# Optimization experiments

Hardware: AMD Instinct MI355X
Metric: run time of the kernel (lower is better)

## Reference

```python
import jax, jax.numpy as jnp
import numpy as np

NUM_TREES = 100
TREE_DEPTH = 5
INPUT_DIM = 256
NUM_CLASSES = 64
BATCH = 8192
NUM_NODES = 2 ** TREE_DEPTH - 1   # 31 decision nodes per tree
NUM_LEAVES = 2 ** TREE_DEPTH      # 32 leaves per tree


def setup_inputs() -> dict:
    key = jax.random.key(0)
    k_x, k_w, k_b, k_l = jax.random.split(key, 4)
    x = jax.random.normal(k_x, (BATCH, INPUT_DIM), dtype=jnp.float32)
    # stacked per-tree decision-node params (torch.randn init)
    node_w = jax.random.normal(k_w, (NUM_TREES, NUM_NODES, INPUT_DIM), dtype=jnp.float32)
    node_b = jax.random.normal(k_b, (NUM_TREES, NUM_NODES), dtype=jnp.float32)
    leaves = jax.random.normal(k_l, (NUM_TREES, NUM_LEAVES, NUM_CLASSES), dtype=jnp.float32)
    return {"x": x, "node_w": node_w, "node_b": node_b, "leaves": leaves}


def reference(x, node_w, node_b, leaves):
    # x: [B, D]; node_w: [T, Nn, D]; node_b: [T, Nn]; leaves: [T, Nl, C]
    T = node_w.shape[0]
    B = x.shape[0]
    depth = int(np.log2(leaves.shape[1]))
    idx = jnp.zeros((T, B), dtype=jnp.int32)
    for _ in range(depth):  # small fixed depth loop
        # gather each sample's routing node per tree: [T, B, D] and [T, B]
        w_g = jnp.take_along_axis(node_w, idx[:, :, None], axis=1)
        b_g = jnp.take_along_axis(node_b, idx, axis=1)
        decisions = jax.nn.sigmoid(jnp.einsum('tbd,bd->tb', w_g, x) + b_g)
        idx = 2 * idx + (decisions <= 0.5).astype(jnp.int32)
    # leaf gather: [T, B, C], then forest average over trees -> [B, C]
    tree_preds = jnp.take_along_axis(leaves, idx[:, :, None], axis=1)
    return jnp.mean(tree_preds, axis=0)
```

## Files before the change

kernel.cpp:

```cpp
#include <hip/hip_runtime.h>


typedef __bf16 bf16;
typedef __attribute__((ext_vector_type(8))) __bf16 bf16x8;
typedef __attribute__((ext_vector_type(4))) float f32x4;
typedef __attribute__((ext_vector_type(4))) unsigned int u32x4;

#define NTREES 100
#define NB     8192
#define ND     256
#define NNODES 31
#define NLEAF  32
#define NCLS   64
#define TAU    2.0e-3f

static __device__ __forceinline__ void gload16(const void* g, void* l) {
    __builtin_amdgcn_global_load_lds(
        (const __attribute__((address_space(1))) void*)g,
        (__attribute__((address_space(3))) void*)l, 16, 0, 0);
}

static __device__ __forceinline__ void split8(const f32x4 v0, const f32x4 v1,
                                              bf16x8* hi, bf16x8* lo) {
    u32x4 b0 = __builtin_bit_cast(u32x4, v0);
    u32x4 b1 = __builtin_bit_cast(u32x4, v1);
    u32x4 h0 = b0 & 0xFFFF0000u;
    u32x4 h1 = b1 & 0xFFFF0000u;
    f32x4 r0 = v0 - __builtin_bit_cast(f32x4, h0);
    f32x4 r1 = v1 - __builtin_bit_cast(f32x4, h1);
    u32x4 c0 = __builtin_bit_cast(u32x4, r0);
    u32x4 c1 = __builtin_bit_cast(u32x4, r1);
    u32x4 hp, lp;
    hp[0] = __builtin_amdgcn_perm(b0[1], b0[0], 0x07060302u);
    hp[1] = __builtin_amdgcn_perm(b0[3], b0[2], 0x07060302u);
    hp[2] = __builtin_amdgcn_perm(b1[1], b1[0], 0x07060302u);
    hp[3] = __builtin_amdgcn_perm(b1[3], b1[2], 0x07060302u);
    lp[0] = __builtin_amdgcn_perm(c0[1], c0[0], 0x07060302u);
    lp[1] = __builtin_amdgcn_perm(c0[3], c0[2], 0x07060302u);
    lp[2] = __builtin_amdgcn_perm(c1[1], c1[0], 0x07060302u);
    lp[3] = __builtin_amdgcn_perm(c1[3], c1[2], 0x07060302u);
    *hi = __builtin_bit_cast(bf16x8, hp);
    *lo = __builtin_bit_cast(bf16x8, lp);
}

static __device__ __forceinline__ int traverse(const float z[16], float* mn_out) {
    float a0 = z[0];
    bool d0 = a0 <= 0.f;
    float a1 = d0 ? z[1] : z[0];
    bool d1 = a1 <= 0.f;
    float a2 = d0 ? (d1 ? z[3] : z[2]) : (d1 ? z[1] : z[0]);
    bool d2 = a2 <= 0.f;
    float m0 = d2 ? z[1] : z[0], m1 = d2 ? z[3] : z[2];
    float m2 = d2 ? z[5] : z[4], m3 = d2 ? z[7] : z[6];
    float p0 = d1 ? m1 : m0, p1 = d1 ? m3 : m2;
    float a3 = d0 ? p1 : p0;
    bool d3 = a3 <= 0.f;
    float n0 = d3 ? z[1] : z[0],  n1 = d3 ? z[3] : z[2];
    float n2 = d3 ? z[5] : z[4],  n3 = d3 ? z[7] : z[6];
    float n4 = d3 ? z[9] : z[8],  n5 = d3 ? z[11] : z[10];
    float n6 = d3 ? z[13] : z[12], n7 = d3 ? z[15] : z[14];
    float q0 = d2 ? n1 : n0, q1 = d2 ? n3 : n2;
    float q2 = d2 ? n5 : n4, q3 = d2 ? n7 : n6;
    float r0 = d1 ? q1 : q0, r1 = d1 ? q3 : q2;
    float a4 = d0 ? r1 : r0;
    bool d4 = a4 <= 0.f;
    *mn_out = fminf(fminf(fminf(fabsf(a0), fabsf(a1)),
                          fminf(fabsf(a2), fabsf(a3))), fabsf(a4));
    return ((int)d0 << 4) | ((int)d1 << 3) | ((int)d2 << 2)
         | ((int)d3 << 1) | (int)d4;
}

__global__ void prep(const float* __restrict__ wf, const float* __restrict__ lv,
                     bf16* __restrict__ wimg, bf16* __restrict__ lv16) {
    if (blockIdx.x < 208) {
        int i = blockIdx.x * 256 + threadIdx.x;
        int oct_g = i & 31;
        int row   = (i >> 5) & 127;
        int tg    = i >> 12;
        int tree  = tg * 8 + (row >> 4), node = row & 15;
        bf16x8 h8, l8;
        if (tree < NTREES) {
            const float* src = wf + ((size_t)tree * NNODES + node) * ND + oct_g * 8;
#pragma unroll
            for (int e = 0; e < 8; ++e) {
                float f = src[e];
                bf16 h = (bf16)f;
                h8[e] = h;
                l8[e] = (bf16)(f - (float)h);
            }
        } else {
#pragma unroll
            for (int e = 0; e < 8; ++e) { h8[e] = (bf16)0.f; l8[e] = (bf16)0.f; }
        }
        int kq = oct_g >> 3, oct = oct_g & 7, cp = oct ^ (row & 7);
        size_t b = (size_t)tg * 65536 + (size_t)kq * 16384 + row * 64 + cp * 8;
        *(bf16x8*)(wimg + b)        = h8;
        *(bf16x8*)(wimg + b + 8192) = l8;
    } else {
        int i = (blockIdx.x - 208) * 256 + threadIdx.x;
        lv16[i] = (bf16)lv[i];
    }
}

__global__ __launch_bounds__(256, 2) void forest_all(
    const float* __restrict__ x,
    const bf16* __restrict__ wimg,
    const float* __restrict__ wf,
    const float* __restrict__ bias,
    unsigned char* __restrict__ idxb)
{
    __shared__ char lds[65536];

    const int tid  = threadIdx.x;
    const int wave = tid >> 6;
    const int lane = tid & 63;
    const int m    = lane & 15;
    const int q    = lane >> 4;

    const int lin  = blockIdx.x + gridDim.x * blockIdx.y;
    const int xcd  = lin & 7;
    const int slot = lin >> 3;
    const int mg   = xcd * 4 + (slot / 13);
    const int tg   = slot % 13;

    f32x4 acc[4][8];
#pragma unroll
    for (int mi = 0; mi < 4; ++mi)
#pragma unroll
        for (int ni = 0; ni < 8; ++ni)
            acc[mi][ni] = (f32x4){0.f, 0.f, 0.f, 0.f};

    const float* xbase = x + (size_t)(mg * 256 + wave * 64 + m) * ND + q * 8;
    const bf16* wsrc = wimg + (size_t)tg * 65536;

#pragma unroll
    for (int j = 0; j < 8; ++j) {
        int idx = j * 256 + tid;
        gload16(wsrc + idx * 8, lds + idx * 16);
    }
    f32x4 raw[4][2];
#pragma unroll
    for (int mi = 0; mi < 4; ++mi) {
        raw[mi][0] = *(const f32x4*)(xbase + mi * 4096);
        raw[mi][1] = *(const f32x4*)(xbase + mi * 4096 + 4);
    }
    __syncthreads();

#pragma unroll
    for (int kq = 0; kq < 4; ++kq) {
        const bf16* bufc = (const bf16*)(lds + (kq & 1) * 32768);
        if (kq < 3) {
            char* bufn = lds + ((kq + 1) & 1) * 32768;
#pragma unroll
            for (int j = 0; j < 8; ++j) {
                int idx = j * 256 + tid;
                gload16(wsrc + (size_t)(kq + 1) * 16384 + idx * 8, bufn + idx * 16);
            }
        }
#pragma unroll
        for (int kkq = 0; kkq < 2; ++kkq) {
            const int kk = kq * 2 + kkq;
            bf16x8 cah[4], cal[4];
#pragma unroll
            for (int mi = 0; mi < 4; ++mi)
                split8(raw[mi][0], raw[mi][1], &cah[mi], &cal[mi]);
            if (kk < 7) {
#pragma unroll
                for (int mi = 0; mi < 4; ++mi) {
                    raw[mi][0] = *(const f32x4*)(xbase + mi * 4096 + (kk + 1) * 32);
                    raw[mi][1] = *(const f32x4*)(xbase + mi * 4096 + (kk + 1) * 32 + 4);
                }
            }
#pragma unroll
            for (int ni = 0; ni < 8; ++ni) {
                const int n  = ni * 16 + m;
                const int cp = (kkq * 4 + q) ^ (m & 7);
                bf16x8 bh = *(const bf16x8*)(bufc + n * 64 + cp * 8);
                bf16x8 bl = *(const bf16x8*)(bufc + 8192 + n * 64 + cp * 8);
#pragma unroll
                for (int mi = 0; mi < 4; ++mi) {
                    acc[mi][ni] = __builtin_amdgcn_mfma_f32_16x16x32_bf16(cal[mi], bh, acc[mi][ni], 0, 0, 0);
                    acc[mi][ni] = __builtin_amdgcn_mfma_f32_16x16x32_bf16(cah[mi], bl, acc[mi][ni], 0, 0, 0);
                    acc[mi][ni] = __builtin_amdgcn_mfma_f32_16x16x32_bf16(cah[mi], bh, acc[mi][ni], 0, 0, 0);
                }
            }
        }
        __syncthreads();
    }

    float biasv[8];
#pragma unroll
    for (int ni = 0; ni < 8; ++ni) {
        int tree = tg * 8 + ni;
        biasv[ni] = (tree < NTREES) ? bias[(size_t)tree * NNODES + m] : 0.f;
    }

    float* ws_ = (float*)lds + wave * 1280;
    const int sg = mg * 256 + wave * 64 + lane;
    unsigned int pk0 = 0, pk1 = 0;
#pragma unroll
    for (int ni = 0; ni < 8; ++ni) {
#pragma unroll
        for (int mi = 0; mi < 4; ++mi)
#pragma unroll
            for (int r = 0; r < 4; ++r)
                ws_[(mi * 16 + q * 4 + r) * 20 + m] = acc[mi][ni][r] + biasv[ni];
        f32x4 z0 = *(f32x4*)&ws_[lane * 20];
        f32x4 z1 = *(f32x4*)&ws_[lane * 20 + 4];
        f32x4 z2 = *(f32x4*)&ws_[lane * 20 + 8];
        f32x4 z3 = *(f32x4*)&ws_[lane * 20 + 12];
        float z[16] = {z0[0], z0[1], z0[2], z0[3], z1[0], z1[1], z1[2], z1[3],
                       z2[0], z2[1], z2[2], z2[3], z3[0], z3[1], z3[2], z3[3]};
        float mn;
        int leaf = traverse(z, &mn);
        const int tree = tg * 8 + ni;
        if (tree < NTREES && mn < TAU) {
            const float* xr = x + (size_t)sg * ND;
            float zc[16];
#pragma unroll
            for (int nd = 0; nd < 16; ++nd) zc[nd] = z[nd];
#pragma unroll
            for (int nd = 0; nd < 16; ++nd) {
                if (fabsf(z[nd]) < TAU) {
                    const float* wr = wf + ((size_t)tree * NNODES + nd) * ND;
                    double s0 = 0.0, s1 = 0.0;
#pragma unroll 4
                    for (int k2 = 0; k2 < 32; ++k2) {
                        f32x4 xv = *(const f32x4*)(xr + k2 * 8);
                        f32x4 wv = *(const f32x4*)(wr + k2 * 8);
                        f32x4 xu = *(const f32x4*)(xr + k2 * 8 + 4);
                        f32x4 wu = *(const f32x4*)(wr + k2 * 8 + 4);
                        s0 += (double)xv[0] * wv[0] + (double)xv[1] * wv[1]
                            + (double)xv[2] * wv[2] + (double)xv[3] * wv[3];
                        s1 += (double)xu[0] * wu[0] + (double)xu[1] * wu[1]
                            + (double)xu[2] * wu[2] + (double)xu[3] * wu[3];
                    }
                    double zt = s0 + s1 + (double)bias[(size_t)tree * NNODES + nd];
                    zc[nd] = (zt <= 0.0) ? -1.f : 1.f;
                }
            }
            float mn2;
            leaf = traverse(zc, &mn2);
        }
        if (ni < 4) pk0 |= (unsigned)leaf << (8 * ni);
        else        pk1 |= (unsigned)leaf << (8 * (ni - 4));
    }
    unsigned char* dst = idxb + (size_t)sg * NTREES + tg * 8;
    *(unsigned int*)dst = pk0;
    if (tg < 12) *(unsigned int*)(dst + 4) = pk1;
}

__global__ void leaf_gather(const unsigned char* __restrict__ idxb,
                            const bf16* __restrict__ lv16,
                            float* __restrict__ out) {
    const int wave = threadIdx.x >> 6;
    const int lane = threadIdx.x & 63;
    const int s = blockIdx.x * 4 + wave;
    unsigned int rw = 0;
    if (lane < 25) rw = *(const unsigned int*)(idxb + (size_t)s * NTREES + lane * 4);
    float acc = 0.f;
#pragma unroll 10
    for (int t = 0; t < NTREES; ++t) {
        unsigned int wrd = __shfl(rw, t >> 2);
        int li = (wrd >> ((t & 3) * 8)) & 255;
        acc += (float)lv16[((size_t)t * NLEAF + li) * NCLS + lane];
    }
    out[(size_t)s * NCLS + lane] = acc * 0.01f;
}

extern "C" void kernel_launch(void* const* d_in, const int* in_sizes, int n_in,
                              void* d_out, int out_size, void* d_ws, size_t ws_size,
                              hipStream_t stream) {
    const float* x  = (const float*)d_in[0];
    const float* nw = (const float*)d_in[1];
    const float* nb = (const float*)d_in[2];
    const float* lv = (const float*)d_in[3];
    float* out = (float*)d_out;

    char* ws = (char*)d_ws;
    bf16* wimg = (bf16*)(ws + 0);
    unsigned char* idxb = (unsigned char*)(ws + 1703936);
    bf16* lv16 = (bf16*)(ws + 2523136);
    if (ws_size < (size_t)2932736) return;

    prep<<<1008, 256, 0, stream>>>(nw, lv, wimg, lv16);
    forest_all<<<dim3(13, 32), 256, 0, stream>>>(x, wimg, nw, nb, idxb);
    leaf_gather<<<NB / 4, 256, 0, stream>>>(idxb, lv16, out);
}
```

Measured before the change: 118.8 us.

## Shrink forest tile to four trees per block to raise occupancy

Each forest_all block now handles 4 trees instead of 8, so 100 trees split evenly into 25 groups with no padded tree. The grid grows to 25x32, and LDS per block and accumulator registers are halved, so three blocks can fit per CU. The software prefetch of x into registers is dropped and x is loaded directly before each split. The cost is that x is loaded and split twice as many times across blocks, and there is no longer any latency hiding for the x loads.

```diff
diff --git a/kernel.cpp b/kernel.cpp
--- a/kernel.cpp
+++ b/kernel.cpp
@@ -72,44 +72,39 @@
 
 __global__ void prep(const float* __restrict__ wf, const float* __restrict__ lv,
                      bf16* __restrict__ wimg, bf16* __restrict__ lv16) {
-    if (blockIdx.x < 208) {
+    if (blockIdx.x < 200) {
         int i = blockIdx.x * 256 + threadIdx.x;
         int oct_g = i & 31;
-        int row   = (i >> 5) & 127;
-        int tg    = i >> 12;
-        int tree  = tg * 8 + (row >> 4), node = row & 15;
+        int row   = (i >> 5) & 63;
+        int tg    = i >> 11;
+        int tree  = tg * 4 + (row >> 4), node = row & 15;
+        const float* src = wf + ((size_t)tree * NNODES + node) * ND + oct_g * 8;
         bf16x8 h8, l8;
-        if (tree < NTREES) {
-            const float* src = wf + ((size_t)tree * NNODES + node) * ND + oct_g * 8;
-#pragma unroll
-            for (int e = 0; e < 8; ++e) {
-                float f = src[e];
-                bf16 h = (bf16)f;
-                h8[e] = h;
-                l8[e] = (bf16)(f - (float)h);
-            }
-        } else {
-#pragma unroll
-            for (int e = 0; e < 8; ++e) { h8[e] = (bf16)0.f; l8[e] = (bf16)0.f; }
+#pragma unroll
+        for (int e = 0; e < 8; ++e) {
+            float f = src[e];
+            bf16 h = (bf16)f;
+            h8[e] = h;
+            l8[e] = (bf16)(f - (float)h);
         }
         int kq = oct_g >> 3, oct = oct_g & 7, cp = oct ^ (row & 7);
-        size_t b = (size_t)tg * 65536 + (size_t)kq * 16384 + row * 64 + cp * 8;
+        size_t b = (size_t)tg * 32768 + (size_t)kq * 8192 + row * 64 + cp * 8;
         *(bf16x8*)(wimg + b)        = h8;
-        *(bf16x8*)(wimg + b + 8192) = l8;
+        *(bf16x8*)(wimg + b + 4096) = l8;
     } else {
-        int i = (blockIdx.x - 208) * 256 + threadIdx.x;
+        int i = (blockIdx.x - 200) * 256 + threadIdx.x;
         lv16[i] = (bf16)lv[i];
     }
 }
 
-__global__ __launch_bounds__(256, 2) void forest_all(
+__global__ __launch_bounds__(256, 3) void forest_all(
     const float* __restrict__ x,
     const bf16* __restrict__ wimg,
     const float* __restrict__ wf,
     const float* __restrict__ bias,
     unsigned char* __restrict__ idxb)
 {
-    __shared__ char lds[65536];
+    __shared__ char lds[32768];
 
     const int tid  = threadIdx.x;
     const int wave = tid >> 6;
@@ -120,41 +115,35 @@
     const int lin  = blockIdx.x + gridDim.x * blockIdx.y;
     const int xcd  = lin & 7;
     const int slot = lin >> 3;
-    const int mg   = xcd * 4 + (slot / 13);
-    const int tg   = slot % 13;
-
-    f32x4 acc[4][8];
+    const int mg   = xcd * 4 + (slot / 25);
+    const int tg   = slot % 25;
+
+    f32x4 acc[4][4];
 #pragma unroll
     for (int mi = 0; mi < 4; ++mi)
 #pragma unroll
-        for (int ni = 0; ni < 8; ++ni)
+        for (int ni = 0; ni < 4; ++ni)
             acc[mi][ni] = (f32x4){0.f, 0.f, 0.f, 0.f};
 
     const float* xbase = x + (size_t)(mg * 256 + wave * 64 + m) * ND + q * 8;
-    const bf16* wsrc = wimg + (size_t)tg * 65536;
-
-#pragma unroll
-    for (int j = 0; j < 8; ++j) {
+    const bf16* wsrc = wimg + (size_t)tg * 32768;
+
+#pragma unroll
+    for (int j = 0; j < 4; ++j) {
         int idx = j * 256 + tid;
         gload16(wsrc + idx * 8, lds + idx * 16);
     }
-    f32x4 raw[4][2];
-#pragma unroll
-    for (int mi = 0; mi < 4; ++mi) {
-        raw[mi][0] = *(const f32x4*)(xbase + mi * 4096);
-        raw[mi][1] = *(const f32x4*)(xbase + mi * 4096 + 4);
-    }
     __syncthreads();
 
 #pragma unroll
     for (int kq = 0; kq < 4; ++kq) {
-        const bf16* bufc = (const bf16*)(lds + (kq & 1) * 32768);
+        const bf16* bufc = (const bf16*)(lds + (kq & 1) * 16384);
         if (kq < 3) {
-            char* bufn = lds + ((kq + 1) & 1) * 32768;
-#pragma unroll
-            for (int j = 0; j < 8; ++j) {
+            char* bufn = lds + ((kq + 1) & 1) * 16384;
+#pragma unroll
+            for (int j = 0; j < 4; ++j) {
                 int idx = j * 256 + tid;
-                gload16(wsrc + (size_t)(kq + 1) * 16384 + idx * 8, bufn + idx * 16);
+                gload16(wsrc + (size_t)(kq + 1) * 8192 + idx * 8, bufn + idx * 16);
             }
         }
 #pragma unroll
@@ -162,21 +151,17 @@
             const int kk = kq * 2 + kkq;
             bf16x8 cah[4], cal[4];
 #pragma unroll
-            for (int mi = 0; mi < 4; ++mi)
-                split8(raw[mi][0], raw[mi][1], &cah[mi], &cal[mi]);
-            if (kk < 7) {
-#pragma unroll
-                for (int mi = 0; mi < 4; ++mi) {
-                    raw[mi][0] = *(const f32x4*)(xbase + mi * 4096 + (kk + 1) * 32);
-                    raw[mi][1] = *(const f32x4*)(xbase + mi * 4096 + (kk + 1) * 32 + 4);
-                }
-            }
-#pragma unroll
-            for (int ni = 0; ni < 8; ++ni) {
+            for (int mi = 0; mi < 4; ++mi) {
+                f32x4 r0 = *(const f32x4*)(xbase + mi * 4096 + kk * 32);
+                f32x4 r1 = *(const f32x4*)(xbase + mi * 4096 + kk * 32 + 4);
+                split8(r0, r1, &cah[mi], &cal[mi]);
+            }
+#pragma unroll
+            for (int ni = 0; ni < 4; ++ni) {
                 const int n  = ni * 16 + m;
                 const int cp = (kkq * 4 + q) ^ (m & 7);
                 bf16x8 bh = *(const bf16x8*)(bufc + n * 64 + cp * 8);
-                bf16x8 bl = *(const bf16x8*)(bufc + 8192 + n * 64 + cp * 8);
+                bf16x8 bl = *(const bf16x8*)(bufc + 4096 + n * 64 + cp * 8);
 #pragma unroll
                 for (int mi = 0; mi < 4; ++mi) {
                     acc[mi][ni] = __builtin_amdgcn_mfma_f32_16x16x32_bf16(cal[mi], bh, acc[mi][ni], 0, 0, 0);
@@ -188,18 +173,16 @@
         __syncthreads();
     }
 
-    float biasv[8];
-#pragma unroll
-    for (int ni = 0; ni < 8; ++ni) {
-        int tree = tg * 8 + ni;
-        biasv[ni] = (tree < NTREES) ? bias[(size_t)tree * NNODES + m] : 0.f;
-    }
+    float biasv[4];
+#pragma unroll
+    for (int ni = 0; ni < 4; ++ni)
+        biasv[ni] = bias[(size_t)(tg * 4 + ni) * NNODES + m];
 
     float* ws_ = (float*)lds + wave * 1280;
     const int sg = mg * 256 + wave * 64 + lane;
-    unsigned int pk0 = 0, pk1 = 0;
-#pragma unroll
-    for (int ni = 0; ni < 8; ++ni) {
+    unsigned int pk = 0;
+#pragma unroll
+    for (int ni = 0; ni < 4; ++ni) {
 #pragma unroll
         for (int mi = 0; mi < 4; ++mi)
 #pragma unroll
@@ -213,8 +196,8 @@
                        z2[0], z2[1], z2[2], z2[3], z3[0], z3[1], z3[2], z3[3]};
         float mn;
         int leaf = traverse(z, &mn);
-        const int tree = tg * 8 + ni;
-        if (tree < NTREES && mn < TAU) {
+        const int tree = tg * 4 + ni;
+        if (mn < TAU) {
             const float* xr = x + (size_t)sg * ND;
             float zc[16];
 #pragma unroll
@@ -242,12 +225,9 @@
             float mn2;
             leaf = traverse(zc, &mn2);
         }
-        if (ni < 4) pk0 |= (unsigned)leaf << (8 * ni);
-        else        pk1 |= (unsigned)leaf << (8 * (ni - 4));
-    }
-    unsigned char* dst = idxb + (size_t)sg * NTREES + tg * 8;
-    *(unsigned int*)dst = pk0;
-    if (tg < 12) *(unsigned int*)(dst + 4) = pk1;
+        pk |= (unsigned)leaf << (8 * ni);
+    }
+    *(unsigned int*)(idxb + (size_t)sg * NTREES + tg * 4) = pk;
 }
 
 __global__ void leaf_gather(const unsigned char* __restrict__ idxb,
@@ -279,11 +259,11 @@
 
     char* ws = (char*)d_ws;
     bf16* wimg = (bf16*)(ws + 0);
-    unsigned char* idxb = (unsigned char*)(ws + 1703936);
-    bf16* lv16 = (bf16*)(ws + 2523136);
-    if (ws_size < (size_t)2932736) return;
-
-    prep<<<1008, 256, 0, stream>>>(nw, lv, wimg, lv16);
-    forest_all<<<dim3(13, 32), 256, 0, stream>>>(x, wimg, nw, nb, idxb);
+    unsigned char* idxb = (unsigned char*)(ws + 1638400);
+    bf16* lv16 = (bf16*)(ws + 2457600);
+    if (ws_size < (size_t)2867200) return;
+
+    prep<<<1000, 256, 0, stream>>>(nw, lv, wimg, lv16);
+    forest_all<<<dim3(25, 32), 256, 0, stream>>>(x, wimg, nw, nb, idxb);
     leaf_gather<<<NB / 4, 256, 0, stream>>>(idxb, lv16, out);
 }
```

Measured after the change: 122.4 us. 1.03x slower.

## Pre-split x into bf16 hi/lo in prep and load fragments directly in GEMM

Applied to the files above, without the earlier changes.

The prep kernel now also splits x into bf16 high and low parts, stored in an MFMA-fragment-friendly layout. The main kernel then loads those fragments directly instead of loading fp32 x and splitting it in-register 13 times redundantly across tree groups. The weight pipeline changes from 4 double-buffered quarters to two 32KB halves loaded with a sync in the middle, which removes overlap between the weight load and compute. The trade-off is extra global write and read traffic for the x images, plus a stall at the midpoint reload.

```diff
diff --git a/kernel.cpp b/kernel.cpp
--- a/kernel.cpp
+++ b/kernel.cpp
@@ -4,7 +4,6 @@
 typedef __bf16 bf16;
 typedef __attribute__((ext_vector_type(8))) __bf16 bf16x8;
 typedef __attribute__((ext_vector_type(4))) float f32x4;
-typedef __attribute__((ext_vector_type(4))) unsigned int u32x4;
 
 #define NTREES 100
 #define NB     8192
@@ -18,29 +17,6 @@
     __builtin_amdgcn_global_load_lds(
         (const __attribute__((address_space(1))) void*)g,
         (__attribute__((address_space(3))) void*)l, 16, 0, 0);
-}
-
-static __device__ __forceinline__ void split8(const f32x4 v0, const f32x4 v1,
-                                              bf16x8* hi, bf16x8* lo) {
-    u32x4 b0 = __builtin_bit_cast(u32x4, v0);
-    u32x4 b1 = __builtin_bit_cast(u32x4, v1);
-    u32x4 h0 = b0 & 0xFFFF0000u;
-    u32x4 h1 = b1 & 0xFFFF0000u;
-    f32x4 r0 = v0 - __builtin_bit_cast(f32x4, h0);
-    f32x4 r1 = v1 - __builtin_bit_cast(f32x4, h1);
-    u32x4 c0 = __builtin_bit_cast(u32x4, r0);
-    u32x4 c1 = __builtin_bit_cast(u32x4, r1);
-    u32x4 hp, lp;
-    hp[0] = __builtin_amdgcn_perm(b0[1], b0[0], 0x07060302u);
-    hp[1] = __builtin_amdgcn_perm(b0[3], b0[2], 0x07060302u);
-    hp[2] = __builtin_amdgcn_perm(b1[1], b1[0], 0x07060302u);
-    hp[3] = __builtin_amdgcn_perm(b1[3], b1[2], 0x07060302u);
-    lp[0] = __builtin_amdgcn_perm(c0[1], c0[0], 0x07060302u);
-    lp[1] = __builtin_amdgcn_perm(c0[3], c0[2], 0x07060302u);
-    lp[2] = __builtin_amdgcn_perm(c1[1], c1[0], 0x07060302u);
-    lp[3] = __builtin_amdgcn_perm(c1[3], c1[2], 0x07060302u);
-    *hi = __builtin_bit_cast(bf16x8, hp);
-    *lo = __builtin_bit_cast(bf16x8, lp);
 }
 
 static __device__ __forceinline__ int traverse(const float z[16], float* mn_out) {
@@ -70,10 +46,28 @@
          | ((int)d3 << 1) | (int)d4;
 }
 
-__global__ void prep(const float* __restrict__ wf, const float* __restrict__ lv,
+__global__ void prep(const float* __restrict__ x, const float* __restrict__ wf,
+                     const float* __restrict__ lv,
+                     bf16* __restrict__ xh, bf16* __restrict__ xl,
                      bf16* __restrict__ wimg, bf16* __restrict__ lv16) {
-    if (blockIdx.x < 208) {
+    if (blockIdx.x < 1024) {
         int i = blockIdx.x * 256 + threadIdx.x;
+        int m  = i & 15;
+        int dq = (i >> 4) & 31;
+        int g  = i >> 9;
+        const float* src = x + (size_t)(g * 16 + m) * ND + dq * 8;
+        bf16x8 h8, l8;
+#pragma unroll
+        for (int e = 0; e < 8; ++e) {
+            float f = src[e];
+            bf16 h = (bf16)f;
+            h8[e] = h;
+            l8[e] = (bf16)(f - (float)h);
+        }
+        *(bf16x8*)(xh + (size_t)i * 8) = h8;
+        *(bf16x8*)(xl + (size_t)i * 8) = l8;
+    } else if (blockIdx.x < 1232) {
+        int i = (blockIdx.x - 1024) * 256 + threadIdx.x;
         int oct_g = i & 31;
         int row   = (i >> 5) & 127;
         int tg    = i >> 12;
@@ -97,14 +91,15 @@
         *(bf16x8*)(wimg + b)        = h8;
         *(bf16x8*)(wimg + b + 8192) = l8;
     } else {
-        int i = (blockIdx.x - 208) * 256 + threadIdx.x;
+        int i = (blockIdx.x - 1232) * 256 + threadIdx.x;
         lv16[i] = (bf16)lv[i];
     }
 }
 
 __global__ __launch_bounds__(256, 2) void forest_all(
+    const bf16* __restrict__ xh, const bf16* __restrict__ xl,
+    const bf16* __restrict__ wimg,
     const float* __restrict__ x,
-    const bf16* __restrict__ wimg,
     const float* __restrict__ wf,
     const float* __restrict__ bias,
     unsigned char* __restrict__ idxb)
@@ -130,63 +125,66 @@
         for (int ni = 0; ni < 8; ++ni)
             acc[mi][ni] = (f32x4){0.f, 0.f, 0.f, 0.f};
 
-    const float* xbase = x + (size_t)(mg * 256 + wave * 64 + m) * ND + q * 8;
+    size_t abase[4];
+#pragma unroll
+    for (int mi = 0; mi < 4; ++mi)
+        abase[mi] = (size_t)(mg * 16 + wave * 4 + mi) * 4096 + lane * 8;
+
     const bf16* wsrc = wimg + (size_t)tg * 65536;
 
 #pragma unroll
-    for (int j = 0; j < 8; ++j) {
+    for (int j = 0; j < 16; ++j) {
         int idx = j * 256 + tid;
         gload16(wsrc + idx * 8, lds + idx * 16);
     }
-    f32x4 raw[4][2];
+    bf16x8 cah[4], cal[4], nah[4], nal[4];
 #pragma unroll
     for (int mi = 0; mi < 4; ++mi) {
-        raw[mi][0] = *(const f32x4*)(xbase + mi * 4096);
-        raw[mi][1] = *(const f32x4*)(xbase + mi * 4096 + 4);
+        cah[mi] = *(const bf16x8*)(xh + abase[mi]);
+        cal[mi] = *(const bf16x8*)(xl + abase[mi]);
     }
     __syncthreads();
 
-#pragma unroll
-    for (int kq = 0; kq < 4; ++kq) {
-        const bf16* bufc = (const bf16*)(lds + (kq & 1) * 32768);
-        if (kq < 3) {
-            char* bufn = lds + ((kq + 1) & 1) * 32768;
-#pragma unroll
-            for (int j = 0; j < 8; ++j) {
+#pragma unroll 1
+    for (int kk = 0; kk < 8; ++kk) {
+        if (kk == 4) {
+            __syncthreads();
+#pragma unroll
+            for (int j = 0; j < 16; ++j) {
                 int idx = j * 256 + tid;
-                gload16(wsrc + (size_t)(kq + 1) * 16384 + idx * 8, bufn + idx * 16);
-            }
-        }
-#pragma unroll
-        for (int kkq = 0; kkq < 2; ++kkq) {
-            const int kk = kq * 2 + kkq;
-            bf16x8 cah[4], cal[4];
+                gload16(wsrc + 32768 + idx * 8, lds + idx * 16);
+            }
+            __syncthreads();
+        }
+        const bf16* bufc = (const bf16*)lds + ((kk >> 1) & 1) * 16384;
+        const int kkq = kk & 1;
+        if (kk < 7) {
+#pragma unroll
+            for (int mi = 0; mi < 4; ++mi) {
+                nah[mi] = *(const bf16x8*)(xh + abase[mi] + (kk + 1) * 512);
+                nal[mi] = *(const bf16x8*)(xl + abase[mi] + (kk + 1) * 512);
+            }
+        }
+#pragma unroll
+        for (int ni = 0; ni < 8; ++ni) {
+            const int n  = ni * 16 + m;
+            const int cp = (kkq * 4 + q) ^ (m & 7);
+            bf16x8 bh = *(const bf16x8*)(bufc + n * 64 + cp * 8);
+            bf16x8 bl = *(const bf16x8*)(bufc + 8192 + n * 64 + cp * 8);
 #pragma unroll
             for (int mi = 0; mi < 4; ++mi)
-                split8(raw[mi][0], raw[mi][1], &cah[mi], &cal[mi]);
-            if (kk < 7) {
-#pragma unroll
-                for (int mi = 0; mi < 4; ++mi) {
-                    raw[mi][0] = *(const f32x4*)(xbase + mi * 4096 + (kk + 1) * 32);
-                    raw[mi][1] = *(const f32x4*)(xbase + mi * 4096 + (kk + 1) * 32 + 4);
-                }
-            }
-#pragma unroll
-            for (int ni = 0; ni < 8; ++ni) {
-                const int n  = ni * 16 + m;
-                const int cp = (kkq * 4 + q) ^ (m & 7);
-                bf16x8 bh = *(const bf16x8*)(bufc + n * 64 + cp * 8);
-                bf16x8 bl = *(const bf16x8*)(bufc + 8192 + n * 64 + cp * 8);
-#pragma unroll
-                for (int mi = 0; mi < 4; ++mi) {
-                    acc[mi][ni] = __builtin_amdgcn_mfma_f32_16x16x32_bf16(cal[mi], bh, acc[mi][ni], 0, 0, 0);
-                    acc[mi][ni] = __builtin_amdgcn_mfma_f32_16x16x32_bf16(cah[mi], bl, acc[mi][ni], 0, 0, 0);
-                    acc[mi][ni] = __builtin_amdgcn_mfma_f32_16x16x32_bf16(cah[mi], bh, acc[mi][ni], 0, 0, 0);
-                }
-            }
-        }
-        __syncthreads();
-    }
+                acc[mi][ni] = __builtin_amdgcn_mfma_f32_16x16x32_bf16(cal[mi], bh, acc[mi][ni], 0, 0, 0);
+#pragma unroll
+            for (int mi = 0; mi < 4; ++mi)
+                acc[mi][ni] = __builtin_amdgcn_mfma_f32_16x16x32_bf16(cah[mi], bl, acc[mi][ni], 0, 0, 0);
+#pragma unroll
+            for (int mi = 0; mi < 4; ++mi)
+                acc[mi][ni] = __builtin_amdgcn_mfma_f32_16x16x32_bf16(cah[mi], bh, acc[mi][ni], 0, 0, 0);
+        }
+#pragma unroll
+        for (int mi = 0; mi < 4; ++mi) { cah[mi] = nah[mi]; cal[mi] = nal[mi]; }
+    }
+    __syncthreads();
 
     float biasv[8];
 #pragma unroll
@@ -278,12 +276,14 @@
     float* out = (float*)d_out;
 
     char* ws = (char*)d_ws;
-    bf16* wimg = (bf16*)(ws + 0);
-    unsigned char* idxb = (unsigned char*)(ws + 1703936);
-    bf16* lv16 = (bf16*)(ws + 2523136);
-    if (ws_size < (size_t)2932736) return;
-
-    prep<<<1008, 256, 0, stream>>>(nw, lv, wimg, lv16);
-    forest_all<<<dim3(13, 32), 256, 0, stream>>>(x, wimg, nw, nb, idxb);
+    bf16* xh   = (bf16*)(ws + 0);
+    bf16* xl   = (bf16*)(ws + 4194304);
+    bf16* wimg = (bf16*)(ws + 8388608);
+    unsigned char* idxb = (unsigned char*)(ws + 10092544);
+    bf16* lv16 = (bf16*)(ws + 10911744);
+    if (ws_size < (size_t)11321344) return;
+
+    prep<<<2032, 256, 0, stream>>>(x, nw, lv, xh, xl, wimg, lv16);
+    forest_all<<<dim3(13, 32), 256, 0, stream>>>(xh, xl, wimg, x, nw, nb, idxb);
     leaf_gather<<<NB / 4, 256, 0, stream>>>(idxb, lv16, out);
 }
```

Result: slower. 128.0 us (+7.7%).
